# Performance work log

Hardware: AMD Instinct MI355X
Metric: run time of the kernel (lower is better)

The kernel has to match this reference:

```python
import jax, jax.numpy as jnp
import numpy as np

T = 0.1          # temperature from CLloss.__init__
PD_EPS = 1e-6    # nn.PairwiseDistance default eps (added to the difference)
NORM_EPS = 1e-12 # F.normalize eps


def setup_inputs() -> dict:
    key = jax.random.key(0)
    k1, k2 = jax.random.split(key)
    embed = jax.random.normal(k1, (16384, 2048), dtype=jnp.float32)
    labels = jax.random.randint(k2, (16384, 20), 0, 2, dtype=jnp.int32)
    return {"embed": embed, "labels": labels}


def reference(embed, labels):
    lab = labels.astype(jnp.float32)
    n = embed.shape[0]
    # F.normalize(embed, dim=-1): x / max(||x||, eps)
    norm = jnp.maximum(jnp.linalg.norm(embed, axis=-1, keepdims=True), NORM_EPS)
    e = embed / norm
    # NOTE: original torch code has `return loss` inside the outer loop, so only
    # anchor i=0 contributes. Faithfully reproduce that.
    # pairwise distance: ||e0 - ej + eps||_2 for j = 1..n-1
    d = jnp.linalg.norm(e[0] - e[1:] + PD_EPS, axis=-1)            # [n-1]
    log_sim = -d / T                                               # log exp(-d/t)
    c = jnp.dot(lab[1:], lab[0])                                   # [n-1] label overlap counts
    Ci = 1e-12 + jnp.sum(c)
    Ei = 1e-12 + jnp.sum(jnp.exp(log_sim))
    # Li = sum_j -(c_j/Ci) * log(exp(-d_j/t)/Ei)
    Li = jnp.sum(-(c / Ci) * (log_sim - jnp.log(Ei)))
    return Li / n
```

## Files before the change

kernel.cpp:

```cpp
#include <hip/hip_runtime.h>
#include <math.h>

#define NROW 16384
#define DIM 2048
#define NLAB 20
#define T_INV 10.0f
#define PD_EPS 1e-6f
#define NORM_EPS 1e-12f

#define BLOCKS 512
#define THREADS 256
#define WPB (THREADS / 64)
#define TOTAL_WAVES (BLOCKS * WPB)
#define FRAG 8


__global__ __launch_bounds__(THREADS) void clloss_main(const float* __restrict__ embed,
                                                       const int* __restrict__ labels,
                                                       float4* __restrict__ partials) {
    const int tid = threadIdx.x;
    const int lane = tid & 63;
    const int wid = tid >> 6;

    const float4* row0 = (const float4*)embed;
    float4 a[FRAG];
#pragma unroll
    for (int it = 0; it < FRAG; ++it) a[it] = row0[it * 64 + lane];

    float s = 0.f, sx = 0.f;
#pragma unroll
    for (int it = 0; it < FRAG; ++it) {
        s  += a[it].x * a[it].x + a[it].y * a[it].y + a[it].z * a[it].z + a[it].w * a[it].w;
        sx += a[it].x + a[it].y + a[it].z + a[it].w;
    }
    for (int o = 32; o; o >>= 1) {
        s  += __shfl_xor(s,  o, 64);
        sx += __shfl_xor(sx, o, 64);
    }
    const float inv0 = 1.0f / fmaxf(sqrtf(s), NORM_EPS);
    const float S_aa = inv0 * inv0 * s + 2.0f * PD_EPS * inv0 * sx
                     + (float)DIM * PD_EPS * PD_EPS;
#pragma unroll
    for (int it = 0; it < FRAG; ++it) {
        a[it].x = a[it].x * inv0 + PD_EPS;
        a[it].y = a[it].y * inv0 + PD_EPS;
        a[it].z = a[it].z * inv0 + PD_EPS;
        a[it].w = a[it].w * inv0 + PD_EPS;
    }
    const float lab0 = (lane < NLAB) ? (float)labels[lane] : 0.f;

    const int gw = blockIdx.x * WPB + wid;
    float acc_e = 0.f, acc_c = 0.f, acc_cl = 0.f;

    int row = 1 + gw;
    float4 cur[FRAG], nxt[FRAG];
    {
        const float4* p = (const float4*)(embed + (size_t)row * DIM);
#pragma unroll
        for (int it = 0; it < FRAG; ++it) cur[it] = p[it * 64 + lane];
    }

    while (row < NROW) {
        const int rnext = row + TOTAL_WAVES;
        const bool has_next = rnext < NROW;
        if (has_next) {
            const float4* q = (const float4*)(embed + (size_t)rnext * DIM);
#pragma unroll
            for (int it = 0; it < FRAG; ++it) nxt[it] = q[it * 64 + lane];
        }
        float c = (lane < NLAB) ? lab0 * (float)labels[row * NLAB + lane] : 0.f;

        float sab = 0.f, sbb = 0.f;
#pragma unroll
        for (int it = 0; it < FRAG; ++it) {
            sab += a[it].x * cur[it].x + a[it].y * cur[it].y
                 + a[it].z * cur[it].z + a[it].w * cur[it].w;
            sbb += cur[it].x * cur[it].x + cur[it].y * cur[it].y
                 + cur[it].z * cur[it].z + cur[it].w * cur[it].w;
        }
        for (int o = 32; o; o >>= 1) {
            sab += __shfl_xor(sab, o, 64);
            sbb += __shfl_xor(sbb, o, 64);
            c   += __shfl_xor(c,   o, 64);
        }
        const float invb = 1.0f / fmaxf(sqrtf(sbb), NORM_EPS);
        const float d2 = fmaxf(S_aa + invb * (invb * sbb - 2.0f * sab), 0.f);
        const float ls = -sqrtf(d2) * T_INV;
        acc_e  += expf(ls);
        acc_c  += c;
        acc_cl += c * ls;

        if (has_next) {
#pragma unroll
            for (int it = 0; it < FRAG; ++it) cur[it] = nxt[it];
        }
        row = rnext;
    }

    __shared__ float wsum[WPB][3];
    if (lane == 0) {
        wsum[wid][0] = acc_e;
        wsum[wid][1] = acc_c;
        wsum[wid][2] = acc_cl;
    }
    __syncthreads();
    if (tid == 0) {
        float4 p;
        p.x = wsum[0][0] + wsum[1][0] + wsum[2][0] + wsum[3][0];
        p.y = wsum[0][1] + wsum[1][1] + wsum[2][1] + wsum[3][1];
        p.z = wsum[0][2] + wsum[1][2] + wsum[2][2] + wsum[3][2];
        p.w = 0.f;
        partials[blockIdx.x] = p;
    }
}

__global__ __launch_bounds__(THREADS) void clloss_final(const float4* __restrict__ partials,
                                                        float* __restrict__ out) {
    __shared__ float red[THREADS / 64][3];
    const int tid = threadIdx.x;
    const int lane = tid & 63, wid = tid >> 6;

    float se = 0.f, sc = 0.f, scl = 0.f;
    for (int i = tid; i < BLOCKS; i += THREADS) {
        float4 p = partials[i];
        se += p.x; sc += p.y; scl += p.z;
    }
    for (int o = 32; o; o >>= 1) {
        se  += __shfl_xor(se,  o, 64);
        sc  += __shfl_xor(sc,  o, 64);
        scl += __shfl_xor(scl, o, 64);
    }
    if (lane == 0) { red[wid][0] = se; red[wid][1] = sc; red[wid][2] = scl; }
    __syncthreads();
    if (tid == 0) {
        se = sc = scl = 0.f;
        for (int w = 0; w < THREADS / 64; ++w) {
            se += red[w][0]; sc += red[w][1]; scl += red[w][2];
        }
        float Ci = 1e-12f + sc;
        float Ei = 1e-12f + se;
        float Li = (sc * logf(Ei) - scl) / Ci;
        out[0] = Li / (float)NROW;
    }
}

extern "C" void kernel_launch(void* const* d_in, const int* in_sizes, int n_in,
                              void* d_out, int out_size, void* d_ws, size_t ws_size,
                              hipStream_t stream) {
    const float* embed = (const float*)d_in[0];
    const int* labels = (const int*)d_in[1];
    float* out = (float*)d_out;
    float4* partials = (float4*)d_ws;

    clloss_main<<<BLOCKS, THREADS, 0, stream>>>(embed, labels, partials);
    clloss_final<<<1, THREADS, 0, stream>>>(partials, out);
}
```

Before: 191.1 us.

## Double grid size and fully unroll each wave's fixed four-row workload

Raises the block count from 512 to 1024 and hints occupancy of 4 blocks per CU. The double-buffered while loop is replaced by a fixed two-iteration loop, with each iteration issuing loads for two rows back to back, so each wave has two rows of loads in flight at once. With 4096 waves and 16383 rows, each wave handles at most four rows. Out-of-range second rows are clamped to row 0 and masked from the sums. The aim is more memory parallelism and less loop and prefetch overhead in a bandwidth-bound streaming read, at the cost of higher register pressure. The code assumes the row count never exceeds four times the wave count.

```diff
diff --git a/kernel.cpp b/kernel.cpp
--- a/kernel.cpp
+++ b/kernel.cpp
@@ -8,16 +8,16 @@
 #define PD_EPS 1e-6f
 #define NORM_EPS 1e-12f
 
-#define BLOCKS 512
+#define BLOCKS 1024
 #define THREADS 256
 #define WPB (THREADS / 64)
 #define TOTAL_WAVES (BLOCKS * WPB)
 #define FRAG 8
 
 
-__global__ __launch_bounds__(THREADS) void clloss_main(const float* __restrict__ embed,
-                                                       const int* __restrict__ labels,
-                                                       float4* __restrict__ partials) {
+__global__ __launch_bounds__(THREADS, 4) void clloss_main(const float* __restrict__ embed,
+                                                          const int* __restrict__ labels,
+                                                          float4* __restrict__ partials) {
     const int tid = threadIdx.x;
     const int lane = tid & 63;
     const int wid = tid >> 6;
@@ -52,49 +52,60 @@
     const int gw = blockIdx.x * WPB + wid;
     float acc_e = 0.f, acc_c = 0.f, acc_cl = 0.f;
 
-    int row = 1 + gw;
-    float4 cur[FRAG], nxt[FRAG];
-    {
-        const float4* p = (const float4*)(embed + (size_t)row * DIM);
 #pragma unroll
-        for (int it = 0; it < FRAG; ++it) cur[it] = p[it * 64 + lane];
-    }
+    for (int half = 0; half < 2; ++half) {
+        const int rA = 1 + gw + half * 2 * TOTAL_WAVES;
+        const int rB = rA + TOTAL_WAVES;
+        const bool vB = rB < NROW;
+        const int rBc = vB ? rB : 0;
 
-    while (row < NROW) {
-        const int rnext = row + TOTAL_WAVES;
-        const bool has_next = rnext < NROW;
-        if (has_next) {
-            const float4* q = (const float4*)(embed + (size_t)rnext * DIM);
+        const float4* pA = (const float4*)(embed + (size_t)rA * DIM);
+        const float4* pB = (const float4*)(embed + (size_t)rBc * DIM);
+
+        float4 bA[FRAG], bB[FRAG];
 #pragma unroll
-            for (int it = 0; it < FRAG; ++it) nxt[it] = q[it * 64 + lane];
-        }
-        float c = (lane < NLAB) ? lab0 * (float)labels[row * NLAB + lane] : 0.f;
+        for (int it = 0; it < FRAG; ++it) bA[it] = pA[it * 64 + lane];
+#pragma unroll
+        for (int it = 0; it < FRAG; ++it) bB[it] = pB[it * 64 + lane];
 
-        float sab = 0.f, sbb = 0.f;
+        float cA = (lane < NLAB) ? lab0 * (float)labels[rA * NLAB + lane] : 0.f;
+        float cB = (lane < NLAB) ? lab0 * (float)labels[rBc * NLAB + lane] : 0.f;
+
+        float sabA = 0.f, sbbA = 0.f, sabB = 0.f, sbbB = 0.f;
 #pragma unroll
         for (int it = 0; it < FRAG; ++it) {
-            sab += a[it].x * cur[it].x + a[it].y * cur[it].y
-                 + a[it].z * cur[it].z + a[it].w * cur[it].w;
-            sbb += cur[it].x * cur[it].x + cur[it].y * cur[it].y
-                 + cur[it].z * cur[it].z + cur[it].w * cur[it].w;
+            sabA += a[it].x * bA[it].x + a[it].y * bA[it].y
+                  + a[it].z * bA[it].z + a[it].w * bA[it].w;
+            sbbA += bA[it].x * bA[it].x + bA[it].y * bA[it].y
+                  + bA[it].z * bA[it].z + bA[it].w * bA[it].w;
+            sabB += a[it].x * bB[it].x + a[it].y * bB[it].y
+                  + a[it].z * bB[it].z + a[it].w * bB[it].w;
+            sbbB += bB[it].x * bB[it].x + bB[it].y * bB[it].y
+                  + bB[it].z * bB[it].z + bB[it].w * bB[it].w;
         }
         for (int o = 32; o; o >>= 1) {
-            sab += __shfl_xor(sab, o, 64);
-            sbb += __shfl_xor(sbb, o, 64);
-            c   += __shfl_xor(c,   o, 64);
+            sabA += __shfl_xor(sabA, o, 64);
+            sbbA += __shfl_xor(sbbA, o, 64);
+            cA   += __shfl_xor(cA,   o, 64);
+            sabB += __shfl_xor(sabB, o, 64);
+            sbbB += __shfl_xor(sbbB, o, 64);
+            cB   += __shfl_xor(cB,   o, 64);
         }
-        const float invb = 1.0f / fmaxf(sqrtf(sbb), NORM_EPS);
-        const float d2 = fmaxf(S_aa + invb * (invb * sbb - 2.0f * sab), 0.f);
-        const float ls = -sqrtf(d2) * T_INV;
-        acc_e  += expf(ls);
-        acc_c  += c;
-        acc_cl += c * ls;
+        const float invA = 1.0f / fmaxf(sqrtf(sbbA), NORM_EPS);
+        const float d2A = fmaxf(S_aa + invA * (invA * sbbA - 2.0f * sabA), 0.f);
+        const float lsA = -sqrtf(d2A) * T_INV;
+        const float invB = 1.0f / fmaxf(sqrtf(sbbB), NORM_EPS);
+        const float d2B = fmaxf(S_aa + invB * (invB * sbbB - 2.0f * sabB), 0.f);
+        const float lsB = -sqrtf(d2B) * T_INV;
 
-        if (has_next) {
-#pragma unroll
-            for (int it = 0; it < FRAG; ++it) cur[it] = nxt[it];
+        acc_e  += expf(lsA);
+        acc_c  += cA;
+        acc_cl += cA * lsA;
+        if (vB) {
+            acc_e  += expf(lsB);
+            acc_c  += cB;
+            acc_cl += cB * lsB;
         }
-        row = rnext;
     }
 
     __shared__ float wsum[WPB][3];
```

Result: slower. 200.8 us (+5.1%).
